# Performance work log

Hardware: AMD Instinct MI355X
Metric: run time of the kernel (lower is better)

Reference implementation:

```python
import jax, jax.numpy as jnp
import numpy as np
from jax import lax

N_T, N_CAPS, CAP_DIM = 8, 16, 16
EPS = 1e-6


def setup_inputs() -> dict:
    key = jax.random.key(0)
    k1, k2 = jax.random.split(key)
    B, H, W = 4, 64, 64
    C = N_T * N_CAPS * CAP_DIM  # 2048
    z = jax.random.normal(k1, (B, C, H, W), dtype=jnp.float32)
    u = jax.random.normal(k2, (B, C, H, W), dtype=jnp.float32)
    weight = jnp.ones((1, 1, 3, 3, 1), dtype=jnp.float32)  # Conv3d (O,I,kT,kD,kS), init ones
    beta = jnp.ones((1,), dtype=jnp.float32)  # correlated_mean_beta, mu_init=1.0
    return {"z": z, "u": u, "weight": weight, "beta": beta}


def reference(z, u, weight, beta):
    B, C, H, W = u.shape
    hw = H * W
    # (B, n_t, n_caps, cap_dim, hw) -> (B, n_caps, n_t, cap_dim, hw) -> (B*n_caps, 1, n_t, cap_dim, hw)
    u_caps = u.reshape(B, N_T, N_CAPS, CAP_DIM, hw)
    u_caps = jnp.transpose(u_caps, (0, 2, 1, 3, 4))
    u_caps = u_caps.reshape(-1, 1, N_T, CAP_DIM, hw)
    u_sq = u_caps * u_caps
    # circular pad over transform and cap_dim axes to keep 'same' size with 3x3x1 kernel
    padded = jnp.pad(u_sq, ((0, 0), (0, 0), (1, 1), (1, 1), (0, 0)), mode="wrap")
    v = lax.conv_general_dilated(
        padded, weight, window_strides=(1, 1, 1), padding="VALID",
        dimension_numbers=("NCDHW", "OIDHW", "NCDHW"),
    )  # (B*n_caps, 1, n_t, cap_dim, hw)
    v = v.reshape(B, N_CAPS, N_T, CAP_DIM, hw)
    v = jnp.transpose(v, (0, 2, 1, 3, 4)).reshape(z.shape)
    std = lax.rsqrt(v + EPS)
    s = (z + beta) * std
    return s
```

## Files before the change

### kernel.cpp

```cpp
#include <hip/hip_runtime.h>

#define N_T 8
#define N_CAPS 16
#define CAP_DIM 16
#define HW 4096
#define P_TILE 64
#define EPS 1e-6f

__global__ __launch_bounds__(256) void caps_norm_kernel(
    const float* __restrict__ z, const float* __restrict__ u,
    const float* __restrict__ w, const float* __restrict__ beta,
    float* __restrict__ out)
{
    __shared__ float lds[128 * P_TILE];

    const int tid = threadIdx.x;
    const int bid = blockIdx.x;
    const int ptile = bid & 63;
    const int c     = (bid >> 6) & 15;
    const int b     = bid >> 10;
    const int p0    = ptile * P_TILE;

    float W9[9];
#pragma unroll
    for (int i = 0; i < 9; ++i) W9[i] = w[i];
    const float bet = beta[0];

    const size_t base_b = (size_t)b * 2048 * HW;

#pragma unroll
    for (int k = 0; k < 8; ++k) {
        int s = tid + k * 256;
        int r = s >> 4;
        int q = s & 15;
        int t = r >> 4, d = r & 15;
        int ch = t * 256 + c * 16 + d;
        const float4 v = *(const float4*)(u + base_b + (size_t)ch * HW + p0 + q * 4);
        float4 sq;
        sq.x = v.x * v.x; sq.y = v.y * v.y; sq.z = v.z * v.z; sq.w = v.w * v.w;
        *(float4*)(lds + r * P_TILE + q * 4) = sq;
    }
    __syncthreads();

    const float4* L = (const float4*)lds;

#pragma unroll
    for (int k = 0; k < 8; ++k) {
        int s = tid + k * 256;
        int r = s >> 4;
        int q = s & 15;
        int t = r >> 4, d = r & 15;

        float ax = 0.f, ay = 0.f, az = 0.f, aw = 0.f;
#pragma unroll
        for (int i = 0; i < 3; ++i) {
            int tt = (t + i + 7) & 7;
#pragma unroll
            for (int j = 0; j < 3; ++j) {
                int dd = (d + j + 15) & 15;
                float ww = W9[i * 3 + j];
                float4 a = L[((tt << 4) + dd) * 16 + q];
                ax += ww * a.x; ay += ww * a.y; az += ww * a.z; aw += ww * a.w;
            }
        }

        int ch = t * 256 + c * 16 + d;
        size_t gidx = base_b + (size_t)ch * HW + p0 + q * 4;
        const float4 z4 = *(const float4*)(z + gidx);
        float4 o;
        o.x = (z4.x + bet) * rsqrtf(ax + EPS);
        o.y = (z4.y + bet) * rsqrtf(ay + EPS);
        o.z = (z4.z + bet) * rsqrtf(az + EPS);
        o.w = (z4.w + bet) * rsqrtf(aw + EPS);
        *(float4*)(out + gidx) = o;
    }
}

extern "C" void kernel_launch(void* const* d_in, const int* in_sizes, int n_in,
                              void* d_out, int out_size, void* d_ws, size_t ws_size,
                              hipStream_t stream) {
    const float* z    = (const float*)d_in[0];
    const float* u    = (const float*)d_in[1];
    const float* w    = (const float*)d_in[2];
    const float* beta = (const float*)d_in[3];
    float* out = (float*)d_out;

    caps_norm_kernel<<<dim3(4096), dim3(256), 0, stream>>>(z, u, w, beta, out);
}
```

Before: 317.5 us.

## Halve pixel tile, pad LDS rows, prefetch z, use nontemporal output stores

Halves the pixel tile per block to 32 and doubles the grid, so each block uses less LDS and more blocks can be resident. LDS rows are padded to 36 floats to cut bank conflicts in the 3x3 stencil reads. All z loads are issued before the stencil compute so their latency overlaps it, and outputs are written with nontemporal stores to avoid cache pollution. In exchange, each block's 128-byte row segments are shorter, there are more blocks to schedule, and the held z values raise register pressure.

Result: slower. 334.5 us (+5.3%).

```diff
diff --git a/kernel.cpp b/kernel.cpp
--- a/kernel.cpp
+++ b/kernel.cpp
@@ -4,21 +4,24 @@
 #define N_CAPS 16
 #define CAP_DIM 16
 #define HW 4096
-#define P_TILE 64
+#define P_TILE 32
+#define ROW_F 36
 #define EPS 1e-6f
+
+typedef float vfloat4 __attribute__((ext_vector_type(4)));
 
 __global__ __launch_bounds__(256) void caps_norm_kernel(
     const float* __restrict__ z, const float* __restrict__ u,
     const float* __restrict__ w, const float* __restrict__ beta,
     float* __restrict__ out)
 {
-    __shared__ float lds[128 * P_TILE];
+    __shared__ float lds[128 * ROW_F];
 
     const int tid = threadIdx.x;
     const int bid = blockIdx.x;
-    const int ptile = bid & 63;
-    const int c     = (bid >> 6) & 15;
-    const int b     = bid >> 10;
+    const int ptile = bid & 127;
+    const int c     = (bid >> 7) & 15;
+    const int b     = bid >> 11;
     const int p0    = ptile * P_TILE;
 
     float W9[9];
@@ -29,29 +32,38 @@
     const size_t base_b = (size_t)b * 2048 * HW;
 
 #pragma unroll
-    for (int k = 0; k < 8; ++k) {
+    for (int k = 0; k < 4; ++k) {
         int s = tid + k * 256;
-        int r = s >> 4;
-        int q = s & 15;
+        int r = s >> 3;
+        int q = s & 7;
         int t = r >> 4, d = r & 15;
         int ch = t * 256 + c * 16 + d;
-        const float4 v = *(const float4*)(u + base_b + (size_t)ch * HW + p0 + q * 4);
-        float4 sq;
-        sq.x = v.x * v.x; sq.y = v.y * v.y; sq.z = v.z * v.z; sq.w = v.w * v.w;
-        *(float4*)(lds + r * P_TILE + q * 4) = sq;
+        const vfloat4 v = *(const vfloat4*)(u + base_b + (size_t)ch * HW + p0 + q * 4);
+        *(vfloat4*)(lds + r * ROW_F + q * 4) = v * v;
     }
     __syncthreads();
 
-    const float4* L = (const float4*)lds;
+    vfloat4 z4[4];
+    size_t gidx[4];
+#pragma unroll
+    for (int k = 0; k < 4; ++k) {
+        int s = tid + k * 256;
+        int r = s >> 3;
+        int q = s & 7;
+        int t = r >> 4, d = r & 15;
+        int ch = t * 256 + c * 16 + d;
+        gidx[k] = base_b + (size_t)ch * HW + p0 + q * 4;
+        z4[k] = *(const vfloat4*)(z + gidx[k]);
+    }
 
 #pragma unroll
-    for (int k = 0; k < 8; ++k) {
+    for (int k = 0; k < 4; ++k) {
         int s = tid + k * 256;
-        int r = s >> 4;
-        int q = s & 15;
+        int r = s >> 3;
+        int q = s & 7;
         int t = r >> 4, d = r & 15;
 
-        float ax = 0.f, ay = 0.f, az = 0.f, aw = 0.f;
+        vfloat4 acc = (vfloat4)0.f;
 #pragma unroll
         for (int i = 0; i < 3; ++i) {
             int tt = (t + i + 7) & 7;
@@ -59,20 +71,17 @@
             for (int j = 0; j < 3; ++j) {
                 int dd = (d + j + 15) & 15;
                 float ww = W9[i * 3 + j];
-                float4 a = L[((tt << 4) + dd) * 16 + q];
-                ax += ww * a.x; ay += ww * a.y; az += ww * a.z; aw += ww * a.w;
+                const vfloat4 a = *(const vfloat4*)(lds + ((tt << 4) + dd) * ROW_F + q * 4);
+                acc += ww * a;
             }
         }
 
-        int ch = t * 256 + c * 16 + d;
-        size_t gidx = base_b + (size_t)ch * HW + p0 + q * 4;
-        const float4 z4 = *(const float4*)(z + gidx);
-        float4 o;
-        o.x = (z4.x + bet) * rsqrtf(ax + EPS);
-        o.y = (z4.y + bet) * rsqrtf(ay + EPS);
-        o.z = (z4.z + bet) * rsqrtf(az + EPS);
-        o.w = (z4.w + bet) * rsqrtf(aw + EPS);
-        *(float4*)(out + gidx) = o;
+        vfloat4 o;
+        o.x = (z4[k].x + bet) * rsqrtf(acc.x + EPS);
+        o.y = (z4[k].y + bet) * rsqrtf(acc.y + EPS);
+        o.z = (z4[k].z + bet) * rsqrtf(acc.z + EPS);
+        o.w = (z4[k].w + bet) * rsqrtf(acc.w + EPS);
+        __builtin_nontemporal_store(o, (vfloat4*)(out + gidx[k]));
     }
 }
 
@@ -85,5 +94,5 @@
     const float* beta = (const float*)d_in[3];
     float* out = (float*)d_out;
 
-    caps_norm_kernel<<<dim3(4096), dim3(256), 0, stream>>>(z, u, w, beta, out);
+    caps_norm_kernel<<<dim3(8192), dim3(256), 0, stream>>>(z, u, w, beta, out);
 }
```
